# Kernel optimization log

Measured on AMD Instinct MI355X. Metric: run time of the kernel, lower is better.

Reference implementation:

```python
import jax, jax.numpy as jnp
import numpy as np

B, T, N, SD, D, HYP, EMB = 128, 256, 8, 200, 64, 64, 32

def _ln(x, g, b, eps=1e-5):
    mu = jnp.mean(x, -1, keepdims=True)
    v = jnp.mean((x - mu) ** 2, -1, keepdims=True)
    return (x - mu) * jax.lax.rsqrt(v + eps) * g + b

def setup_inputs():
    key = jax.random.key(0)
    ks = iter(jax.random.split(key, 64))
    def p(shape, scale=0.05):
        return (jax.random.normal(next(ks), shape) * scale).astype(jnp.float32)
    n, sd, d, hyp, emb = N, SD, D, HYP, EMB
    return dict(
        qvals=p((B, T, n), 1.0), states=p((B, T, sd), 1.0), hidden_state=p((B, T, n, d), 1.0),
        enc_w1=p((sd, d)), enc_b1=p((d,)), enc_w2=p((d, d)), enc_b2=p((d,)),
        wq=p((d, d)), bq=p((d,)), wk=p((d, d)), bk=p((d,)), wv=p((d, d)), bv=p((d,)),
        wo=p((d, d)), bo=p((d,)),
        ln1_g=jnp.ones((d,), jnp.float32), ln1_b=jnp.zeros((d,), jnp.float32),
        ffn_w1=p((d, d)), ffn_b1=p((d,)), ffn_w2=p((d, d)), ffn_b2=p((d,)),
        ln2_g=jnp.ones((d,), jnp.float32), ln2_b=jnp.zeros((d,), jnp.float32),
        fc2ni_w=p((n, d, n - 1)), fc2ni_b=p((n, n - 1)),
        norm_g=jnp.ones((n - 1,), jnp.float32), norm_b=jnp.zeros((n - 1,), jnp.float32),
        w1a=p((2 * d, hyp)), b1a=p((hyp,)), w1b=p((hyp, n * emb)), b1b=p((n * emb,)),
        hb1w=p((2 * d, emb)), hb1b=p((emb,)),
        w2a=p((2 * d, hyp)), b2a=p((hyp,)), w2b=p((hyp, emb)), b2b=p((emb,)),
        hb2w1=p((2 * d, emb)), hb2b1=p((emb,)), hb2w2=p((emb, 1)), hb2b2=p((1,)))

def reference(qvals, states, hidden_state, enc_w1, enc_b1, enc_w2, enc_b2,
              wq, bq, wk, bk, wv, bv, wo, bo, ln1_g, ln1_b,
              ffn_w1, ffn_b1, ffn_w2, ffn_b2, ln2_g, ln2_b,
              fc2ni_w, fc2ni_b, norm_g, norm_b,
              w1a, b1a, w1b, b1b, hb1w, hb1b,
              w2a, b2a, w2b, b2b, hb2w1, hb2b1, hb2w2, hb2b2):
    sg = jax.lax.stop_gradient
    b, t, n = qvals.shape
    bt = b * t
    d = hidden_state.shape[-1]
    emb = hb1w.shape[1]
    # Encoder_s: relu(fc1) then tanh(fc2(e)+e)
    s = states.reshape(bt, -1)
    e = jax.nn.relu(s @ enc_w1 + enc_b1)
    enc = jnp.tanh(e @ enc_w2 + enc_b2 + e)                       # (bt, 64)
    # concat detached agent hiddens with detached state embedding -> (bt, n+1, 64)
    h = jnp.concatenate([sg(hidden_state.reshape(bt, n, d)), sg(enc)[:, None, :]], axis=1)
    # transformer block (single-head self-attention + FFN, post-LN)
    q = h @ wq + bq; k = h @ wk + bk; v = h @ wv + bv
    att = jax.nn.softmax(jnp.einsum('bid,bjd->bij', q, k) / jnp.sqrt(jnp.float32(d)), axis=-1)
    h2 = _ln(h + (att @ v) @ wo + bo, ln1_g, ln1_b)
    h3 = _ln(h2 + jax.nn.relu(h2 @ ffn_w1 + ffn_b1) @ ffn_w2 + ffn_b2, ln2_g, ln2_b)
    h_trans = h3[:, :n]                                           # (bt, n, 64)
    ens = jnp.concatenate([enc, sg(h_trans).mean(1)], axis=-1)    # (bt, 128)
    # per-agent fc2_Ni -> LayerNorm -> sigmoid, vectorized over agents
    ni = jnp.einsum('xnd,nde->xne', h_trans, fc2ni_w) + fc2ni_b   # (bt, n, n-1)
    ni = jax.nn.sigmoid(_ln(ni, norm_g, norm_b))
    # insert 1.0 at the diagonal (agent i keeps its own q with weight 1)
    rows = jnp.arange(n)[:, None]; cols = jnp.arange(n)[None, :]
    gidx = jnp.clip(cols - (cols > rows).astype(jnp.int32), 0, n - 2)  # (n, n)
    gathered = jnp.take_along_axis(ni, jnp.broadcast_to(gidx, (bt, n, n)), axis=-1)
    nfull = jnp.where(cols == rows, jnp.float32(1.0), gathered)   # (bt, n, n)
    N_nn = nfull.reshape(b, t, n, n)
    q_ni = (qvals[:, :, None, :] * N_nn).sum(-1).reshape(bt, 1, n)
    # hypernetwork mixing (QMIX)
    ens_d = sg(ens)
    w1 = jnp.abs(jax.nn.relu(ens_d @ w1a + b1a) @ w1b + b1b).reshape(bt, n, emb)
    b1 = (ens_d @ hb1w + hb1b).reshape(bt, 1, emb)
    w2 = jnp.abs(jax.nn.relu(ens @ w2a + b2a) @ w2b + b2b).reshape(bt, emb, 1)
    b2 = (jax.nn.relu(ens @ hb2w1 + hb2b1) @ hb2w2 + hb2b2).reshape(bt, 1, 1)
    hidden = jax.nn.elu(q_ni @ w1 + b1)
    y = (hidden @ w2 + b2).reshape(b, t, 1)
    eye_mask = jnp.broadcast_to(jnp.eye(n, dtype=bool), (b, t, n, n))
    return y, N_nn, eye_mask
```

## Files before the change

kernel.cpp:

```cpp
#include <hip/hip_runtime.h>
#include <hip/hip_bf16.h>

typedef __bf16 bf16x8 __attribute__((ext_vector_type(8)));
typedef __bf16 bf16x4 __attribute__((ext_vector_type(4)));
typedef float f32x4 __attribute__((ext_vector_type(4)));

#define ROWSG 32768
#define RB 6
#define NBLK 5462
#define HPAD 72
#define NN_OFF ((size_t)ROWSG)
#define EYE_OFF ((size_t)ROWSG + (size_t)ROWSG*64)

#define OFF_EW1   0
#define OFF_EW2   14336
#define OFF_WQ    18432
#define OFF_WK    22528
#define OFF_WV    26624
#define OFF_WO    30720
#define OFF_F1    34816
#define OFF_F2    38912
#define OFF_W1A   43008
#define OFF_W1B   51200
#define OFF_HB1W  67584
#define OFF_W2A   71680
#define OFF_W2B   79872
#define OFF_HB2W1 81920
#define OFF_NI    86016
#define WS_TOTAL  94208

__device__ __align__(16) __bf16 g_ws[WS_TOTAL];

#define MFMA16(a,b,c) __builtin_amdgcn_mfma_f32_16x16x32_bf16(a,b,c,0,0,0)

struct TP { const float* src[15]; };

__global__ __launch_bounds__(256) void wtrans(TP tp) {
    const int gid = blockIdx.x * 256 + threadIdx.x;
    if (gid >= WS_TOTAL) return;
    if (gid >= OFF_NI) {
        const int loc = gid - OFF_NI;
        const int nmat = loc >> 10, rem = loc & 1023, e = rem >> 6, k = rem & 63;
        float v = (e < 7) ? tp.src[14][nmat * 448 + k * 7 + e] : 0.f;
        g_ws[gid] = (__bf16)v;
        return;
    }
    const int OFFS[14] = {OFF_EW1, OFF_EW2, OFF_WQ, OFF_WK, OFF_WV, OFF_WO, OFF_F1,
                          OFF_F2, OFF_W1A, OFF_W1B, OFF_HB1W, OFF_W2A, OFF_W2B, OFF_HB2W1};
    const int KPS[14]  = {224, 64, 64, 64, 64, 64, 64, 64, 128, 64, 128, 128, 64, 128};
    const int KRS[14]  = {200, 64, 64, 64, 64, 64, 64, 64, 128, 64, 128, 128, 64, 128};
    const int NS[14]   = {64, 64, 64, 64, 64, 64, 64, 64, 64, 256, 32, 64, 32, 32};
    int m = 0;
#pragma unroll
    for (int i = 1; i < 14; ++i) if (gid >= OFFS[i]) m = i;
    const int loc = gid - OFFS[m];
    const int Kp = KPS[m];
    const int n = loc / Kp;
    const int k = loc - n * Kp;
    float v = 0.f;
    if (k < KRS[m]) v = tp.src[m][(size_t)k * NS[m] + n];
    g_ws[gid] = (__bf16)v;
}

struct MainP {
    const float *qvals, *states, *hid, *eb1, *eb2, *bq, *bk, *bv, *bo,
        *l1g, *l1b, *fb1, *fb2, *l2g, *l2b, *niw, *nib, *ng, *nb,
        *b1a, *b1b, *hb1b, *b2a, *b2b, *hb2b1, *hw2, *hb2b2;
    float* out;
};

__device__ __forceinline__ void proj_ln4(const __bf16* A, const __bf16* WT,
                                         const float* bias, const float* g, const float* bb,
                                         __bf16* H, int w, int quad, int l15) {
    const int mt = w;
    f32x4 acc0 = {0,0,0,0}, acc1 = {0,0,0,0}, acc2 = {0,0,0,0}, acc3 = {0,0,0,0};
#pragma unroll
    for (int ks = 0; ks < 2; ++ks) {
        const int kk = ks * 32 + quad * 8;
        const bf16x8 af = *(const bf16x8*)(A + (mt * 16 + l15) * HPAD + kk);
        acc0 = MFMA16(af, *(const bf16x8*)(WT + (size_t)(0 * 16 + l15) * 64 + kk), acc0);
        acc1 = MFMA16(af, *(const bf16x8*)(WT + (size_t)(1 * 16 + l15) * 64 + kk), acc1);
        acc2 = MFMA16(af, *(const bf16x8*)(WT + (size_t)(2 * 16 + l15) * 64 + kk), acc2);
        acc3 = MFMA16(af, *(const bf16x8*)(WT + (size_t)(3 * 16 + l15) * 64 + kk), acc3);
    }
    float v[4][4], g4[4], b4[4];
#pragma unroll
    for (int nt = 0; nt < 4; ++nt) {
        const int col = nt * 16 + l15;
        const float bo = bias[col];
        g4[nt] = g[col]; b4[nt] = bb[col];
        const f32x4 a = (nt == 0) ? acc0 : (nt == 1) ? acc1 : (nt == 2) ? acc2 : acc3;
#pragma unroll
        for (int r = 0; r < 4; ++r)
            v[nt][r] = a[r] + bo + (float)H[(mt * 16 + quad * 4 + r) * HPAD + col];
    }
#pragma unroll
    for (int r = 0; r < 4; ++r) {
        float s  = v[0][r] + v[1][r] + v[2][r] + v[3][r];
        float s2 = v[0][r]*v[0][r] + v[1][r]*v[1][r] + v[2][r]*v[2][r] + v[3][r]*v[3][r];
#pragma unroll
        for (int off = 1; off < 16; off <<= 1) {
            s  += __shfl_xor(s,  off, 64);
            s2 += __shfl_xor(s2, off, 64);
        }
        const float mu  = s * 0.015625f;
        const float var = s2 * 0.015625f - mu * mu;
        const float rs  = rsqrtf(var + 1e-5f);
#pragma unroll
        for (int nt = 0; nt < 4; ++nt)
            H[(mt * 16 + quad * 4 + r) * HPAD + nt * 16 + l15] =
                (__bf16)((v[nt][r] - mu) * rs * g4[nt] + b4[nt]);
    }
}

__global__ __launch_bounds__(256) void mixer_main(MainP p) {
    __shared__ __align__(16) __bf16 Hb[64 * HPAD];
    __shared__ __align__(16) __bf16 Qb[64 * HPAD];
    __shared__ __align__(16) __bf16 Kb[64 * HPAD];
    __shared__ __align__(16) __bf16 EbU[16 * HPAD];
    __shared__ float  attU[6 * 81];
    __shared__ float  sQv[48];
    __shared__ float  qniL[48];

    __bf16* Sb   = Qb;
    __bf16* W1bS = Qb;
    float*  B1f  = (float*)(Qb + 1536);
    float*  W2f  = (float*)(Qb + 1920);
    float*  T3f  = (float*)(Qb + 2304);
    __bf16* Tb2  = Qb + 2688;
    float*  sNiP = (float*)(Qb + 3840);
    __bf16* ensB = Kb;

    const int blk = blockIdx.x;
    const int bt0 = blk * RB;
    const int t = threadIdx.x;
    const int w = t >> 6, lane = t & 63, quad = lane >> 4, l15 = lane & 15;
    const __bf16* ws = g_ws;

#pragma unroll
    for (int it = 0; it < 3; ++it) {
        const int u = it * 256 + t;
        const int x = u >> 7, rem = u & 127, n = rem >> 4, d4 = (rem & 15) * 4;
        const int bt = bt0 + x;
        const size_t btc = (bt < ROWSG) ? bt : (ROWSG - 1);
        const float4 v4 = *(const float4*)(p.hid + (btc * 512 + n * 64 + d4));
        bf16x4 o; o[0] = (__bf16)v4.x; o[1] = (__bf16)v4.y; o[2] = (__bf16)v4.z; o[3] = (__bf16)v4.w;
        *(bf16x4*)(Hb + (x * 9 + n) * HPAD + d4) = o;
    }
#pragma unroll
    for (int it = 0; it < 2; ++it) {
        const int u = it * 256 + t;
        if (u < 300) {
            const int xr = u / 50, c4 = u - xr * 50;
            const int bt = bt0 + xr;
            const size_t btc = (bt < ROWSG) ? bt : (ROWSG - 1);
            const float4 v4 = *(const float4*)(p.states + btc * 200 + c4 * 4);
            bf16x4 o; o[0] = (__bf16)v4.x; o[1] = (__bf16)v4.y; o[2] = (__bf16)v4.z; o[3] = (__bf16)v4.w;
            *(bf16x4*)(Sb + xr * 224 + c4 * 4) = o;
        }
    }
    if (t < 144) { const int xr = t / 24, c = t - xr * 24; Sb[xr * 224 + 200 + c] = (__bf16)0.0f; }
    if (t < 48) {
        const int bt = bt0 + (t >> 3);
        const size_t btc = (bt < ROWSG) ? bt : (ROWSG - 1);
        sQv[t] = p.qvals[btc * 8 + (t & 7)];
    }
    __syncthreads();

    float e4[4];
    {
        const int n0 = w * 16;
        const int srow = (l15 < RB) ? l15 : (RB - 1);
        f32x4 acc = {0, 0, 0, 0};
        for (int ks = 0; ks < 7; ++ks) {
            const int kk = ks * 32 + quad * 8;
            const bf16x8 af = *(const bf16x8*)(Sb + srow * 224 + kk);
            const bf16x8 bf = *(const bf16x8*)(ws + OFF_EW1 + (size_t)(n0 + l15) * 224 + kk);
            acc = MFMA16(af, bf, acc);
        }
        const float b1 = p.eb1[n0 + l15];
#pragma unroll
        for (int r = 0; r < 4; ++r) {
            const float ev = fmaxf(acc[r] + b1, 0.f);
            e4[r] = ev;
            EbU[(quad * 4 + r) * HPAD + n0 + l15] = (__bf16)ev;
        }
    }
    __syncthreads();

    {
        const int n0 = w * 16;
        f32x4 acc = {0, 0, 0, 0};
#pragma unroll
        for (int ks = 0; ks < 2; ++ks) {
            const int kk = ks * 32 + quad * 8;
            const bf16x8 af = *(const bf16x8*)(EbU + l15 * HPAD + kk);
            const bf16x8 bf = *(const bf16x8*)(ws + OFF_EW2 + (size_t)(n0 + l15) * 64 + kk);
            acc = MFMA16(af, bf, acc);
        }
        const float b2 = p.eb2[n0 + l15];
#pragma unroll
        for (int r = 0; r < 4; ++r) {
            const int xr = quad * 4 + r;
            if (xr < RB) {
                const float ev = tanhf(acc[r] + e4[r] + b2);
                Hb[(xr * 9 + 8) * HPAD + n0 + l15] = (__bf16)ev;
                EbU[(8 + xr) * HPAD + n0 + l15] = (__bf16)ev;
            }
        }
    }
    __syncthreads();

    for (int it = 0; it < 8; ++it) {
        const int j = w + 4 * it;
        const int mat = j >> 4, r16 = j & 15, mt = r16 >> 2, nt = r16 & 3;
        const __bf16* wt = ws + (mat == 0 ? OFF_WQ : OFF_WK);
        const float* bias = (mat == 0 ? p.bq : p.bk);
        __bf16* dst = (mat == 0 ? Qb : Kb);
        f32x4 acc = {0, 0, 0, 0};
#pragma unroll
        for (int ks = 0; ks < 2; ++ks) {
            const int kk = ks * 32 + quad * 8;
            const bf16x8 af = *(const bf16x8*)(Hb + (mt * 16 + l15) * HPAD + kk);
            const bf16x8 bf = *(const bf16x8*)(wt + (size_t)(nt * 16 + l15) * 64 + kk);
            acc = MFMA16(af, bf, acc);
        }
        const float bv = bias[nt * 16 + l15];
#pragma unroll
        for (int r = 0; r < 4; ++r)
            dst[(mt * 16 + quad * 4 + r) * HPAD + nt * 16 + l15] = (__bf16)(acc[r] + bv);
    }
    __syncthreads();

    for (int xi = 0; xi < 2; ++xi) {
        const int x = w * 2 + xi;
        if (x >= RB) continue;
        {
            const int arow = (x * 9 + l15) * HPAD;
            f32x4 acc = {0, 0, 0, 0};
#pragma unroll
            for (int ks = 0; ks < 2; ++ks) {
                const int kk = ks * 32 + quad * 8;
                const bf16x8 qa = *(const bf16x8*)(Qb + arow + kk);
                const bf16x8 kb = *(const bf16x8*)(Kb + arow + kk);
                acc = MFMA16(qa, kb, acc);
            }
#pragma unroll
            for (int r = 0; r < 4; ++r) {
                const int i = quad * 4 + r;
                float s = (l15 < 9) ? acc[r] * 0.125f : -3.0e38f;
                float m = s;
#pragma unroll
                for (int off = 1; off < 16; off <<= 1) m = fmaxf(m, __shfl_xor(m, off, 64));
                float e = (l15 < 9) ? __expf(s - m) : 0.f;
                float sum = e;
#pragma unroll
                for (int off = 1; off < 16; off <<= 1) sum += __shfl_xor(sum, off, 64);
                const float pv = e / sum;
                if (i < 9 && l15 < 9) attU[x * 81 + i * 9 + l15] = pv;
            }
        }
        {
            float vreg[9];
#pragma unroll
            for (int jj = 0; jj < 9; ++jj) vreg[jj] = (float)Hb[(x * 9 + jj) * HPAD + lane];
#pragma unroll
            for (int i = 0; i < 9; ++i) {
                float a = 0.f;
#pragma unroll
                for (int jj = 0; jj < 9; ++jj) a += attU[x * 81 + i * 9 + jj] * vreg[jj];
                Kb[(x * 9 + i) * HPAD + lane] = (__bf16)a;
            }
        }
    }
    __syncthreads();

    for (int it = 0; it < 4; ++it) {
        const int j = w + 4 * it;
        const int mt = j >> 2, nt = j & 3;
        f32x4 acc = {0, 0, 0, 0};
#pragma unroll
        for (int ks = 0; ks < 2; ++ks) {
            const int kk = ks * 32 + quad * 8;
            const bf16x8 af = *(const bf16x8*)(Kb + (mt * 16 + l15) * HPAD + kk);
            const bf16x8 bf = *(const bf16x8*)(ws + OFF_WV + (size_t)(nt * 16 + l15) * 64 + kk);
            acc = MFMA16(af, bf, acc);
        }
        const float bv = p.bv[nt * 16 + l15];
#pragma unroll
        for (int r = 0; r < 4; ++r)
            Qb[(mt * 16 + quad * 4 + r) * HPAD + nt * 16 + l15] = (__bf16)(acc[r] + bv);
    }
    __syncthreads();

    proj_ln4(Qb, ws + OFF_WO, p.bo, p.l1g, p.l1b, Hb, w, quad, l15);
    __syncthreads();

    for (int it = 0; it < 4; ++it) {
        const int j = w + 4 * it;
        const int mt = j >> 2, nt = j & 3;
        f32x4 acc = {0, 0, 0, 0};
#pragma unroll
        for (int ks = 0; ks < 2; ++ks) {
            const int kk = ks * 32 + quad * 8;
            const bf16x8 af = *(const bf16x8*)(Hb + (mt * 16 + l15) * HPAD + kk);
            const bf16x8 bf = *(const bf16x8*)(ws + OFF_F1 + (size_t)(nt * 16 + l15) * 64 + kk);
            acc = MFMA16(af, bf, acc);
        }
        const float fb = p.fb1[nt * 16 + l15];
#pragma unroll
        for (int r = 0; r < 4; ++r)
            Kb[(mt * 16 + quad * 4 + r) * HPAD + nt * 16 + l15] = (__bf16)fmaxf(acc[r] + fb, 0.f);
    }
    __syncthreads();

    proj_ln4(Kb, ws + OFF_F2, p.fb2, p.l2g, p.l2b, Hb, w, quad, l15);
    __syncthreads();

    {
        const int id = t;
#pragma unroll
        for (int it = 0; it < 2; ++it) {
            const int u = it * 256 + id;
            if (u < 384) {
                const int x = u >> 6, col = u & 63;
                float s = 0.f;
#pragma unroll
                for (int i = 0; i < 8; ++i) s += (float)Hb[(x * 9 + i) * HPAD + col];
                ensB[x * 136 + 64 + col] = (__bf16)(s * 0.125f);
                ensB[x * 136 + col] = EbU[(8 + x) * HPAD + col];
            }
        }
    }
    for (int jn = 0; jn < 2; ++jn) {
        const int n = w * 2 + jn;
        const int l15c = (l15 < RB) ? l15 : (RB - 1);
        f32x4 acc = {0, 0, 0, 0};
#pragma unroll
        for (int ks = 0; ks < 2; ++ks) {
            const int kk = ks * 32 + quad * 8;
            const bf16x8 af = *(const bf16x8*)(Hb + (l15c * 9 + n) * HPAD + kk);
            const bf16x8 bf = *(const bf16x8*)(ws + OFF_NI + n * 1024 + (size_t)l15 * 64 + kk);
            acc = MFMA16(af, bf, acc);
        }
#pragma unroll
        for (int r = 0; r < 4; ++r) {
            const int x = quad * 4 + r;
            const float av = (l15 < 7) ? (acc[r] + p.nib[n * 7 + l15]) : 0.f;
            float s1 = av;
            s1 += __shfl_xor(s1, 1, 64); s1 += __shfl_xor(s1, 2, 64);
            s1 += __shfl_xor(s1, 4, 64); s1 += __shfl_xor(s1, 8, 64);
            const float mu = s1 * (1.f / 7.f);
            float d0 = (l15 < 7) ? (av - mu) : 0.f;
            float s2 = d0 * d0;
            s2 += __shfl_xor(s2, 1, 64); s2 += __shfl_xor(s2, 2, 64);
            s2 += __shfl_xor(s2, 4, 64); s2 += __shfl_xor(s2, 8, 64);
            const float rs = rsqrtf(s2 * (1.f / 7.f) + 1e-5f);
            if (x < RB && l15 < 7) {
                const float vv = (av - mu) * rs * p.ng[l15] + p.nb[l15];
                sNiP[(x * 8 + n) * 7 + l15] = 1.f / (1.f + __expf(-vv));
            }
        }
    }
    __syncthreads();

    {
        float* Nf = attU;
#pragma unroll
        for (int it = 0; it < 2; ++it) {
            const int u = it * 256 + t;
            if (u < 384) {
                const int x = u >> 6, rem = u & 63, i = rem >> 3, jj = rem & 7;
                const float nf = (i == jj) ? 1.f : sNiP[(x * 8 + i) * 7 + jj - (jj > i ? 1 : 0)];
                const int bt = bt0 + x;
                if (bt < ROWSG) {
                    p.out[NN_OFF + (size_t)bt * 64 + rem] = nf;
                    p.out[EYE_OFF + (size_t)bt * 64 + rem] = (i == jj) ? 1.f : 0.f;
                }
                Nf[x * 64 + rem] = nf;
            }
        }
    }
    __syncthreads();

    if (t < 192) {
        const float* Nf = attU;
        const int pr = t >> 2, q4 = t & 3;
        const int x = pr >> 3, i = pr & 7;
        const int j0 = q4 * 2;
        float s = sQv[x * 8 + j0] * Nf[x * 64 + i * 8 + j0] +
                  sQv[x * 8 + j0 + 1] * Nf[x * 64 + i * 8 + j0 + 1];
        s += __shfl_xor(s, 1, 64);
        s += __shfl_xor(s, 2, 64);
        if (q4 == 0) qniL[x * 8 + i] = s;
    }
    {
        const int n0 = w * 16;
#pragma unroll
        for (int m2 = 0; m2 < 2; ++m2) {
            const __bf16* wt = ws + (m2 == 0 ? OFF_W1A : OFF_W2A);
            const float* bias = m2 == 0 ? p.b1a : p.b2a;
            __bf16* dst = m2 == 0 ? EbU : Tb2;
            f32x4 acc = {0, 0, 0, 0};
#pragma unroll
            for (int ks = 0; ks < 4; ++ks) {
                const int kk = ks * 32 + quad * 8;
                const bf16x8 af = *(const bf16x8*)(ensB + l15 * 136 + kk);
                const bf16x8 bf = *(const bf16x8*)(wt + (size_t)(n0 + l15) * 128 + kk);
                acc = MFMA16(af, bf, acc);
            }
            const float bb = bias[n0 + l15];
#pragma unroll
            for (int r = 0; r < 4; ++r)
                dst[(quad * 4 + r) * HPAD + n0 + l15] = (__bf16)fmaxf(acc[r] + bb, 0.f);
        }
    }
    __syncthreads();

    for (int it = 0; it < 6; ++it) {
        const int j = w + 4 * it;
        if (j >= 22) continue;
        int mode, n0, Kp, ksteps, aStride;
        const __bf16 *A, *WT; const float* bias;
        if (j < 16)      { mode = 0; n0 = j * 16;        A = EbU;  aStride = HPAD; WT = ws + OFF_W1B;   bias = p.b1b;  Kp = 64;  ksteps = 2; }
        else if (j < 18) { mode = 1; n0 = (j - 16) * 16; A = ensB; aStride = 136;  WT = ws + OFF_HB1W;  bias = p.hb1b; Kp = 128; ksteps = 4; }
        else if (j < 20) { mode = 2; n0 = (j - 18) * 16; A = Tb2;  aStride = HPAD; WT = ws + OFF_W2B;   bias = p.b2b;  Kp = 64;  ksteps = 2; }
        else             { mode = 3; n0 = (j - 20) * 16; A = ensB; aStride = 136;  WT = ws + OFF_HB2W1; bias = p.hb2b1;Kp = 128; ksteps = 4; }
        f32x4 acc = {0, 0, 0, 0};
        for (int ks = 0; ks < ksteps; ++ks) {
            const int kk = ks * 32 + quad * 8;
            const bf16x8 af = *(const bf16x8*)(A + l15 * aStride + kk);
            const bf16x8 bf = *(const bf16x8*)(WT + (size_t)(n0 + l15) * Kp + kk);
            acc = MFMA16(af, bf, acc);
        }
        const float bb = bias[n0 + l15];
#pragma unroll
        for (int r = 0; r < 4; ++r) {
            const int xr = quad * 4 + r;
            if (xr < RB) {
                const float val = acc[r] + bb;
                if (mode == 0)      W1bS[xr * 256 + n0 + l15] = (__bf16)fabsf(val);
                else if (mode == 1) B1f[xr * 32 + n0 + l15] = val;
                else if (mode == 2) W2f[xr * 32 + n0 + l15] = fabsf(val);
                else                T3f[xr * 32 + n0 + l15] = fmaxf(val, 0.f);
            }
        }
    }
    __syncthreads();

    if (t < 96) {
        const int x = t >> 4, sub = t & 15;
        float pp = 0.f, pb = 0.f;
#pragma unroll
        for (int h2i = 0; h2i < 2; ++h2i) {
            const int e = sub + h2i * 16;
            float a = B1f[x * 32 + e];
#pragma unroll
            for (int i = 0; i < 8; ++i) a += qniL[x * 8 + i] * (float)W1bS[x * 256 + i * 32 + e];
            const float hid = a > 0.f ? a : (__expf(a) - 1.f);
            pp += hid * W2f[x * 32 + e];
            pb += T3f[x * 32 + e] * p.hw2[e];
        }
#pragma unroll
        for (int off = 1; off < 16; off <<= 1) {
            pp += __shfl_xor(pp, off, 64);
            pb += __shfl_xor(pb, off, 64);
        }
        const int bt = bt0 + x;
        if (sub == 0 && bt < ROWSG) p.out[bt] = pp + pb + p.hb2b2[0];
    }
}

extern "C" void kernel_launch(void* const* d_in, const int* in_sizes, int n_in,
                              void* d_out, int out_size, void* d_ws, size_t ws_size,
                              hipStream_t stream) {
    TP tp;
    tp.src[0]  = (const float*)d_in[3];
    tp.src[1]  = (const float*)d_in[5];
    tp.src[2]  = (const float*)d_in[7];
    tp.src[3]  = (const float*)d_in[9];
    tp.src[4]  = (const float*)d_in[11];
    tp.src[5]  = (const float*)d_in[13];
    tp.src[6]  = (const float*)d_in[17];
    tp.src[7]  = (const float*)d_in[19];
    tp.src[8]  = (const float*)d_in[27];
    tp.src[9]  = (const float*)d_in[29];
    tp.src[10] = (const float*)d_in[31];
    tp.src[11] = (const float*)d_in[33];
    tp.src[12] = (const float*)d_in[35];
    tp.src[13] = (const float*)d_in[37];
    tp.src[14] = (const float*)d_in[23];
    wtrans<<<(WS_TOTAL + 255) / 256, 256, 0, stream>>>(tp);

    MainP p;
    p.qvals = (const float*)d_in[0];
    p.states = (const float*)d_in[1];
    p.hid = (const float*)d_in[2];
    p.eb1 = (const float*)d_in[4];
    p.eb2 = (const float*)d_in[6];
    p.bq = (const float*)d_in[8];
    p.bk = (const float*)d_in[10];
    p.bv = (const float*)d_in[12];
    p.bo = (const float*)d_in[14];
    p.l1g = (const float*)d_in[15];
    p.l1b = (const float*)d_in[16];
    p.fb1 = (const float*)d_in[18];
    p.fb2 = (const float*)d_in[20];
    p.l2g = (const float*)d_in[21];
    p.l2b = (const float*)d_in[22];
    p.niw = (const float*)d_in[23];
    p.nib = (const float*)d_in[24];
    p.ng = (const float*)d_in[25];
    p.nb = (const float*)d_in[26];
    p.b1a = (const float*)d_in[28];
    p.b1b = (const float*)d_in[30];
    p.hb1b = (const float*)d_in[32];
    p.b2a = (const float*)d_in[34];
    p.b2b = (const float*)d_in[36];
    p.hb2b1 = (const float*)d_in[38];
    p.hw2 = (const float*)d_in[39];
    p.hb2b2 = (const float*)d_in[40];
    p.out = (float*)d_out;

    mixer_main<<<NBLK, 256, 0, stream>>>(p);
}
```

Baseline: 397.6 us.

## Give each wave whole row tiles in transformer GEMMs and drop barriers

Reassigns MFMA tiles so each wave owns a 16-row M tile and computes all four N tiles, for Q/K, V, FFN1 and the hypernet W1b GEMMs. The A fragment is then loaded once per k-step, and because each wave only reads its own rows, several __syncthreads between chained GEMMs and proj_ln4 can be removed. It also pads the attention matrix to stride 12 so rows can be read with float4, and fuses the qvals-by-N reduction into the N-matrix write using shuffles. The risks are higher register pressure from holding four to eight accumulators per wave, and a correctness dependency on the row ownership in proj_ln4 matching the new layout.

Result: slower. 454.5 us (+14.3%).

```diff
diff --git a/kernel.cpp b/kernel.cpp
--- a/kernel.cpp
+++ b/kernel.cpp
@@ -118,9 +118,7 @@
     __shared__ __align__(16) __bf16 Qb[64 * HPAD];
     __shared__ __align__(16) __bf16 Kb[64 * HPAD];
     __shared__ __align__(16) __bf16 EbU[16 * HPAD];
-    __shared__ float  attU[6 * 81];
-    __shared__ float  sQv[48];
-    __shared__ float  qniL[48];
+    __shared__ __align__(16) float  attU[6 * 108];
 
     __bf16* Sb   = Qb;
     __bf16* W1bS = Qb;
@@ -129,6 +127,7 @@
     float*  T3f  = (float*)(Qb + 2304);
     __bf16* Tb2  = Qb + 2688;
     float*  sNiP = (float*)(Qb + 3840);
+    float*  qniL = (float*)(Qb + 4512);
     __bf16* ensB = Kb;
 
     const int blk = blockIdx.x;
@@ -160,11 +159,6 @@
         }
     }
     if (t < 144) { const int xr = t / 24, c = t - xr * 24; Sb[xr * 224 + 200 + c] = (__bf16)0.0f; }
-    if (t < 48) {
-        const int bt = bt0 + (t >> 3);
-        const size_t btc = (bt < ROWSG) ? bt : (ROWSG - 1);
-        sQv[t] = p.qvals[btc * 8 + (t & 7)];
-    }
     __syncthreads();
 
     float e4[4];
@@ -211,24 +205,29 @@
     }
     __syncthreads();
 
-    for (int it = 0; it < 8; ++it) {
-        const int j = w + 4 * it;
-        const int mat = j >> 4, r16 = j & 15, mt = r16 >> 2, nt = r16 & 3;
-        const __bf16* wt = ws + (mat == 0 ? OFF_WQ : OFF_WK);
-        const float* bias = (mat == 0 ? p.bq : p.bk);
-        __bf16* dst = (mat == 0 ? Qb : Kb);
-        f32x4 acc = {0, 0, 0, 0};
+    {
+        f32x4 aq[4] = {{0,0,0,0},{0,0,0,0},{0,0,0,0},{0,0,0,0}};
+        f32x4 ak[4] = {{0,0,0,0},{0,0,0,0},{0,0,0,0},{0,0,0,0}};
 #pragma unroll
         for (int ks = 0; ks < 2; ++ks) {
             const int kk = ks * 32 + quad * 8;
-            const bf16x8 af = *(const bf16x8*)(Hb + (mt * 16 + l15) * HPAD + kk);
-            const bf16x8 bf = *(const bf16x8*)(wt + (size_t)(nt * 16 + l15) * 64 + kk);
-            acc = MFMA16(af, bf, acc);
-        }
-        const float bv = bias[nt * 16 + l15];
-#pragma unroll
-        for (int r = 0; r < 4; ++r)
-            dst[(mt * 16 + quad * 4 + r) * HPAD + nt * 16 + l15] = (__bf16)(acc[r] + bv);
+            const bf16x8 af = *(const bf16x8*)(Hb + (w * 16 + l15) * HPAD + kk);
+#pragma unroll
+            for (int nt = 0; nt < 4; ++nt) {
+                aq[nt] = MFMA16(af, *(const bf16x8*)(ws + OFF_WQ + (size_t)(nt * 16 + l15) * 64 + kk), aq[nt]);
+                ak[nt] = MFMA16(af, *(const bf16x8*)(ws + OFF_WK + (size_t)(nt * 16 + l15) * 64 + kk), ak[nt]);
+            }
+        }
+#pragma unroll
+        for (int nt = 0; nt < 4; ++nt) {
+            const float bq = p.bq[nt * 16 + l15], bk = p.bk[nt * 16 + l15];
+#pragma unroll
+            for (int r = 0; r < 4; ++r) {
+                const int row = w * 16 + quad * 4 + r;
+                Qb[row * HPAD + nt * 16 + l15] = (__bf16)(aq[nt][r] + bq);
+                Kb[row * HPAD + nt * 16 + l15] = (__bf16)(ak[nt][r] + bk);
+            }
+        }
     }
     __syncthreads();
 
@@ -257,7 +256,7 @@
 #pragma unroll
                 for (int off = 1; off < 16; off <<= 1) sum += __shfl_xor(sum, off, 64);
                 const float pv = e / sum;
-                if (i < 9 && l15 < 9) attU[x * 81 + i * 9 + l15] = pv;
+                if (i < 9 && l15 < 9) attU[x * 108 + i * 12 + l15] = pv;
             }
         }
         {
@@ -266,62 +265,62 @@
             for (int jj = 0; jj < 9; ++jj) vreg[jj] = (float)Hb[(x * 9 + jj) * HPAD + lane];
 #pragma unroll
             for (int i = 0; i < 9; ++i) {
-                float a = 0.f;
-#pragma unroll
-                for (int jj = 0; jj < 9; ++jj) a += attU[x * 81 + i * 9 + jj] * vreg[jj];
+                const float4 a0 = *(const float4*)(attU + x * 108 + i * 12);
+                const float4 a1 = *(const float4*)(attU + x * 108 + i * 12 + 4);
+                const float a8 = attU[x * 108 + i * 12 + 8];
+                const float a = a0.x * vreg[0] + a0.y * vreg[1] + a0.z * vreg[2] + a0.w * vreg[3]
+                              + a1.x * vreg[4] + a1.y * vreg[5] + a1.z * vreg[6] + a1.w * vreg[7]
+                              + a8 * vreg[8];
                 Kb[(x * 9 + i) * HPAD + lane] = (__bf16)a;
             }
         }
     }
     __syncthreads();
 
-    for (int it = 0; it < 4; ++it) {
-        const int j = w + 4 * it;
-        const int mt = j >> 2, nt = j & 3;
-        f32x4 acc = {0, 0, 0, 0};
+    {
+        f32x4 acc[4] = {{0,0,0,0},{0,0,0,0},{0,0,0,0},{0,0,0,0}};
 #pragma unroll
         for (int ks = 0; ks < 2; ++ks) {
             const int kk = ks * 32 + quad * 8;
-            const bf16x8 af = *(const bf16x8*)(Kb + (mt * 16 + l15) * HPAD + kk);
-            const bf16x8 bf = *(const bf16x8*)(ws + OFF_WV + (size_t)(nt * 16 + l15) * 64 + kk);
-            acc = MFMA16(af, bf, acc);
-        }
-        const float bv = p.bv[nt * 16 + l15];
-#pragma unroll
-        for (int r = 0; r < 4; ++r)
-            Qb[(mt * 16 + quad * 4 + r) * HPAD + nt * 16 + l15] = (__bf16)(acc[r] + bv);
-    }
-    __syncthreads();
-
+            const bf16x8 af = *(const bf16x8*)(Kb + (w * 16 + l15) * HPAD + kk);
+#pragma unroll
+            for (int nt = 0; nt < 4; ++nt)
+                acc[nt] = MFMA16(af, *(const bf16x8*)(ws + OFF_WV + (size_t)(nt * 16 + l15) * 64 + kk), acc[nt]);
+        }
+#pragma unroll
+        for (int nt = 0; nt < 4; ++nt) {
+            const float bv = p.bv[nt * 16 + l15];
+#pragma unroll
+            for (int r = 0; r < 4; ++r)
+                Qb[(w * 16 + quad * 4 + r) * HPAD + nt * 16 + l15] = (__bf16)(acc[nt][r] + bv);
+        }
+    }
     proj_ln4(Qb, ws + OFF_WO, p.bo, p.l1g, p.l1b, Hb, w, quad, l15);
-    __syncthreads();
-
-    for (int it = 0; it < 4; ++it) {
-        const int j = w + 4 * it;
-        const int mt = j >> 2, nt = j & 3;
-        f32x4 acc = {0, 0, 0, 0};
+    {
+        f32x4 acc[4] = {{0,0,0,0},{0,0,0,0},{0,0,0,0},{0,0,0,0}};
 #pragma unroll
         for (int ks = 0; ks < 2; ++ks) {
             const int kk = ks * 32 + quad * 8;
-            const bf16x8 af = *(const bf16x8*)(Hb + (mt * 16 + l15) * HPAD + kk);
-            const bf16x8 bf = *(const bf16x8*)(ws + OFF_F1 + (size_t)(nt * 16 + l15) * 64 + kk);
-            acc = MFMA16(af, bf, acc);
-        }
-        const float fb = p.fb1[nt * 16 + l15];
-#pragma unroll
-        for (int r = 0; r < 4; ++r)
-            Kb[(mt * 16 + quad * 4 + r) * HPAD + nt * 16 + l15] = (__bf16)fmaxf(acc[r] + fb, 0.f);
-    }
-    __syncthreads();
-
+            const bf16x8 af = *(const bf16x8*)(Hb + (w * 16 + l15) * HPAD + kk);
+#pragma unroll
+            for (int nt = 0; nt < 4; ++nt)
+                acc[nt] = MFMA16(af, *(const bf16x8*)(ws + OFF_F1 + (size_t)(nt * 16 + l15) * 64 + kk), acc[nt]);
+        }
+#pragma unroll
+        for (int nt = 0; nt < 4; ++nt) {
+            const float fb = p.fb1[nt * 16 + l15];
+#pragma unroll
+            for (int r = 0; r < 4; ++r)
+                Kb[(w * 16 + quad * 4 + r) * HPAD + nt * 16 + l15] = (__bf16)fmaxf(acc[nt][r] + fb, 0.f);
+        }
+    }
     proj_ln4(Kb, ws + OFF_F2, p.fb2, p.l2g, p.l2b, Hb, w, quad, l15);
     __syncthreads();
 
     {
-        const int id = t;
 #pragma unroll
         for (int it = 0; it < 2; ++it) {
-            const int u = it * 256 + id;
+            const int u = it * 256 + t;
             if (u < 384) {
                 const int x = u >> 6, col = u & 63;
                 float s = 0.f;
@@ -365,7 +364,6 @@
     __syncthreads();
 
     {
-        float* Nf = attU;
 #pragma unroll
         for (int it = 0; it < 2; ++it) {
             const int u = it * 256 + t;
@@ -373,59 +371,71 @@
                 const int x = u >> 6, rem = u & 63, i = rem >> 3, jj = rem & 7;
                 const float nf = (i == jj) ? 1.f : sNiP[(x * 8 + i) * 7 + jj - (jj > i ? 1 : 0)];
                 const int bt = bt0 + x;
+                const size_t btc = (bt < ROWSG) ? bt : (ROWSG - 1);
                 if (bt < ROWSG) {
                     p.out[NN_OFF + (size_t)bt * 64 + rem] = nf;
                     p.out[EYE_OFF + (size_t)bt * 64 + rem] = (i == jj) ? 1.f : 0.f;
                 }
-                Nf[x * 64 + rem] = nf;
-            }
-        }
-    }
-    __syncthreads();
-
-    if (t < 192) {
-        const float* Nf = attU;
-        const int pr = t >> 2, q4 = t & 3;
-        const int x = pr >> 3, i = pr & 7;
-        const int j0 = q4 * 2;
-        float s = sQv[x * 8 + j0] * Nf[x * 64 + i * 8 + j0] +
-                  sQv[x * 8 + j0 + 1] * Nf[x * 64 + i * 8 + j0 + 1];
-        s += __shfl_xor(s, 1, 64);
-        s += __shfl_xor(s, 2, 64);
-        if (q4 == 0) qniL[x * 8 + i] = s;
+                float s = p.qvals[btc * 8 + jj] * nf;
+                s += __shfl_xor(s, 1, 64); s += __shfl_xor(s, 2, 64); s += __shfl_xor(s, 4, 64);
+                if (jj == 0) qniL[x * 8 + i] = s;
+            }
+        }
     }
     {
         const int n0 = w * 16;
-#pragma unroll
-        for (int m2 = 0; m2 < 2; ++m2) {
-            const __bf16* wt = ws + (m2 == 0 ? OFF_W1A : OFF_W2A);
-            const float* bias = m2 == 0 ? p.b1a : p.b2a;
-            __bf16* dst = m2 == 0 ? EbU : Tb2;
-            f32x4 acc = {0, 0, 0, 0};
-#pragma unroll
-            for (int ks = 0; ks < 4; ++ks) {
-                const int kk = ks * 32 + quad * 8;
-                const bf16x8 af = *(const bf16x8*)(ensB + l15 * 136 + kk);
-                const bf16x8 bf = *(const bf16x8*)(wt + (size_t)(n0 + l15) * 128 + kk);
-                acc = MFMA16(af, bf, acc);
-            }
-            const float bb = bias[n0 + l15];
-#pragma unroll
-            for (int r = 0; r < 4; ++r)
-                dst[(quad * 4 + r) * HPAD + n0 + l15] = (__bf16)fmaxf(acc[r] + bb, 0.f);
-        }
-    }
-    __syncthreads();
-
-    for (int it = 0; it < 6; ++it) {
+        f32x4 ac1 = {0,0,0,0}, ac2 = {0,0,0,0};
+#pragma unroll
+        for (int ks = 0; ks < 4; ++ks) {
+            const int kk = ks * 32 + quad * 8;
+            const bf16x8 af = *(const bf16x8*)(ensB + l15 * 136 + kk);
+            ac1 = MFMA16(af, *(const bf16x8*)(ws + OFF_W1A + (size_t)(n0 + l15) * 128 + kk), ac1);
+            ac2 = MFMA16(af, *(const bf16x8*)(ws + OFF_W2A + (size_t)(n0 + l15) * 128 + kk), ac2);
+        }
+        const float b1 = p.b1a[n0 + l15], b2 = p.b2a[n0 + l15];
+#pragma unroll
+        for (int r = 0; r < 4; ++r) {
+            EbU[(quad * 4 + r) * HPAD + n0 + l15] = (__bf16)fmaxf(ac1[r] + b1, 0.f);
+            Tb2[(quad * 4 + r) * HPAD + n0 + l15] = (__bf16)fmaxf(ac2[r] + b2, 0.f);
+        }
+    }
+    __syncthreads();
+
+    {
+        f32x4 acc[4] = {{0,0,0,0},{0,0,0,0},{0,0,0,0},{0,0,0,0}};
+#pragma unroll
+        for (int ks = 0; ks < 2; ++ks) {
+            const int kk = ks * 32 + quad * 8;
+            const bf16x8 af = *(const bf16x8*)(EbU + l15 * HPAD + kk);
+#pragma unroll
+            for (int nt = 0; nt < 4; ++nt) {
+                const int n0 = (w * 4 + nt) * 16;
+                acc[nt] = MFMA16(af, *(const bf16x8*)(ws + OFF_W1B + (size_t)(n0 + l15) * 64 + kk), acc[nt]);
+            }
+        }
+#pragma unroll
+        for (int nt = 0; nt < 4; ++nt) {
+            const int n0 = (w * 4 + nt) * 16;
+            const float bb = p.b1b[n0 + l15];
+#pragma unroll
+            for (int r = 0; r < 4; ++r) {
+                const int xr = quad * 4 + r;
+                if (xr < RB) W1bS[xr * 256 + n0 + l15] = (__bf16)fabsf(acc[nt][r] + bb);
+            }
+        }
+    }
+#pragma unroll
+    for (int it = 0; it < 2; ++it) {
         const int j = w + 4 * it;
-        if (j >= 22) continue;
-        int mode, n0, Kp, ksteps, aStride;
-        const __bf16 *A, *WT; const float* bias;
-        if (j < 16)      { mode = 0; n0 = j * 16;        A = EbU;  aStride = HPAD; WT = ws + OFF_W1B;   bias = p.b1b;  Kp = 64;  ksteps = 2; }
-        else if (j < 18) { mode = 1; n0 = (j - 16) * 16; A = ensB; aStride = 136;  WT = ws + OFF_HB1W;  bias = p.hb1b; Kp = 128; ksteps = 4; }
-        else if (j < 20) { mode = 2; n0 = (j - 18) * 16; A = Tb2;  aStride = HPAD; WT = ws + OFF_W2B;   bias = p.b2b;  Kp = 64;  ksteps = 2; }
-        else             { mode = 3; n0 = (j - 20) * 16; A = ensB; aStride = 136;  WT = ws + OFF_HB2W1; bias = p.hb2b1;Kp = 128; ksteps = 4; }
+        if (j >= 6) continue;
+        const int mode = (j < 2) ? 1 : (j < 4) ? 2 : 3;
+        const int n0 = (j & 1) * 16;
+        const __bf16* A  = (mode == 2) ? Tb2 : ensB;
+        const int aStride = (mode == 2) ? HPAD : 136;
+        const __bf16* WT = ws + ((mode == 1) ? OFF_HB1W : (mode == 2) ? OFF_W2B : OFF_HB2W1);
+        const float* bias = (mode == 1) ? p.hb1b : (mode == 2) ? p.b2b : p.hb2b1;
+        const int Kp = (mode == 2) ? 64 : 128;
+        const int ksteps = (mode == 2) ? 2 : 4;
         f32x4 acc = {0, 0, 0, 0};
         for (int ks = 0; ks < ksteps; ++ks) {
             const int kk = ks * 32 + quad * 8;
@@ -439,8 +449,7 @@
             const int xr = quad * 4 + r;
             if (xr < RB) {
                 const float val = acc[r] + bb;
-                if (mode == 0)      W1bS[xr * 256 + n0 + l15] = (__bf16)fabsf(val);
-                else if (mode == 1) B1f[xr * 32 + n0 + l15] = val;
+                if (mode == 1)      B1f[xr * 32 + n0 + l15] = val;
                 else if (mode == 2) W2f[xr * 32 + n0 + l15] = fabsf(val);
                 else                T3f[xr * 32 + n0 + l15] = fmaxf(val, 0.f);
             }
```
